# Kernel tuning notes

Hardware: AMD Instinct MI355X
Metric: run time of the kernel (lower is better)

## Reference

```python
import jax, jax.numpy as jnp
import numpy as np

RADIUS = 1
N_POINTS = 8


def lbp(x, radius=RADIUS, n_points=N_POINTS):
    """skimage-style 'default' LBP applied per pixel of an NCHW batch.

    For each of P points on a circle of radius R, bilinearly sample the
    neighbor (zero outside the image, matching skimage's constant mode),
    compare >= center, and bit-pack with weights 2**p.
    Offsets follow skimage: row = -R*sin(theta), col = R*cos(theta).
    """
    B, C, H, W = x.shape
    angles = 2.0 * np.pi * np.arange(n_points) / n_points
    drs = np.round(-radius * np.sin(angles), 8)
    dcs = np.round(radius * np.cos(angles), 8)
    pad = int(np.ceil(radius)) + 1
    xp = jnp.pad(x, ((0, 0), (0, 0), (pad, pad), (pad, pad)))  # zeros outside

    code = jnp.zeros_like(x)
    for p in range(n_points):
        dr, dc = float(drs[p]), float(dcs[p])
        r0, c0 = int(np.floor(dr)), int(np.floor(dc))
        fr, fc = dr - r0, dc - c0  # fractional parts in [0,1)

        def win(ri, ci):
            rs, cs = pad + r0 + ri, pad + c0 + ci
            return jax.lax.slice(xp, (0, 0, rs, cs), (B, C, rs + H, cs + W))

        # bilinear sample of the shifted neighborhood (constant-0 boundary)
        v = ((1 - fr) * (1 - fc) * win(0, 0)
             + (1 - fr) * fc * win(0, 1)
             + fr * (1 - fc) * win(1, 0)
             + fr * fc * win(1, 1))
        code = code + float(2 ** p) * (v >= x).astype(x.dtype)
    return code


def setup_inputs() -> dict:
    key = jax.random.key(0)
    x = jax.random.uniform(key, (16, 64, 224, 224), dtype=jnp.float32)
    return {"x": x}


def reference(x):
    return lbp(x)
```

## Files before the change

### kernel.cpp

```cpp
#include <hip/hip_runtime.h>
#include <math.h>

#define HH 224
#define WW 224
#define PLANES (16 * 64)
#define TILES_X (WW / 4)
#define TILES_PER_PLANE (TILES_X * (HH / 4))
#define TOTAL_THREADS (PLANES * TILES_PER_PLANE)

struct LbpWeights {
    float w1[4];
    float w3[4];
    float w5[4];
    float w7[4];
};

__global__ __launch_bounds__(256) void lbp_kernel(const float* __restrict__ x,
                                                  float* __restrict__ out,
                                                  LbpWeights wt) {
    int tid = blockIdx.x * 256 + threadIdx.x;

    int plane = tid / TILES_PER_PLANE;
    int t = tid - plane * TILES_PER_PLANE;
    int tr = t / TILES_X;
    int tc = t - tr * TILES_X;
    int r0 = tr * 4, c0 = tc * 4;

    const float* pb = x + (size_t)plane * (HH * WW);

    float a[6][6];
    bool cm = (c0 > 0), cp = (c0 + 4 < WW);
#pragma unroll
    for (int i = 0; i < 6; i++) {
        int rr = r0 - 1 + i;
        if (rr >= 0 && rr < HH) {
            const float* rp = pb + rr * WW + c0;
            float4 v = *(const float4*)rp;
            a[i][1] = v.x; a[i][2] = v.y; a[i][3] = v.z; a[i][4] = v.w;
            a[i][0] = cm ? rp[-1] : 0.0f;
            a[i][5] = cp ? rp[4]  : 0.0f;
        } else {
#pragma unroll
            for (int k = 0; k < 6; k++) a[i][k] = 0.0f;
        }
    }

    float* ob = out + (size_t)plane * (HH * WW) + r0 * WW + c0;

#pragma unroll
    for (int j = 0; j < 4; j++) {
        float res[4];
#pragma unroll
        for (int k = 0; k < 4; k++) {
            float ctr = a[j + 1][k + 1];
            float n00 = a[j][k],     n01 = a[j][k + 1],     n02 = a[j][k + 2];
            float n10 = a[j + 1][k],                        n12 = a[j + 1][k + 2];
            float n20 = a[j + 2][k], n21 = a[j + 2][k + 1], n22 = a[j + 2][k + 2];

            float v1, v3, v5, v7;
            {
#pragma clang fp contract(off)
                v1 = ((wt.w1[0] * n01 + wt.w1[1] * n02) + wt.w1[2] * ctr) + wt.w1[3] * n12;
                v3 = ((wt.w3[0] * n00 + wt.w3[1] * n01) + wt.w3[2] * n10) + wt.w3[3] * ctr;
                v5 = ((wt.w5[0] * n10 + wt.w5[1] * ctr) + wt.w5[2] * n20) + wt.w5[3] * n21;
                v7 = ((wt.w7[0] * ctr + wt.w7[1] * n12) + wt.w7[2] * n21) + wt.w7[3] * n22;
            }

            int m = 0;
            m |= (n12 >= ctr) ? 1   : 0;
            m |= (v1  >= ctr) ? 2   : 0;
            m |= (n01 >= ctr) ? 4   : 0;
            m |= (v3  >= ctr) ? 8   : 0;
            m |= (n10 >= ctr) ? 16  : 0;
            m |= (v5  >= ctr) ? 32  : 0;
            m |= (n21 >= ctr) ? 64  : 0;
            m |= (v7  >= ctr) ? 128 : 0;
            res[k] = (float)m;
        }
        *(float4*)(ob + j * WW) = make_float4(res[0], res[1], res[2], res[3]);
    }
}

extern "C" void kernel_launch(void* const* d_in, const int* in_sizes, int n_in,
                              void* d_out, int out_size, void* d_ws, size_t ws_size,
                              hipStream_t stream) {
    (void)in_sizes; (void)n_in; (void)d_ws; (void)ws_size; (void)out_size;
    const float* x = (const float*)d_in[0];
    float* out = (float*)d_out;

    LbpWeights wt;
    float* slots[4] = {wt.w1, wt.w3, wt.w5, wt.w7};
    const int diag_p[4] = {1, 3, 5, 7};
    for (int i = 0; i < 4; i++) {
        int p = diag_p[i];
        double ang = (2.0 * M_PI * (double)p) / 8.0;
        double dr = rint(-sin(ang) * 1e8) / 1e8;
        double dc = rint( cos(ang) * 1e8) / 1e8;
        double r0 = floor(dr), c0 = floor(dc);
        double fr = dr - r0, fc = dc - c0;
        slots[i][0] = (float)((1.0 - fr) * (1.0 - fc));
        slots[i][1] = (float)((1.0 - fr) * fc);
        slots[i][2] = (float)(fr * (1.0 - fc));
        slots[i][3] = (float)(fr * fc);
    }

    const int block = 256;
    const int grid = TOTAL_THREADS / block;
    lbp_kernel<<<grid, block, 0, stream>>>(x, out, wt);
}
```

Baseline: 371.8 us.

## Stream 28-row strips per thread with rolling row buffer and nontemporal stores

Each thread now walks a 4-wide, 28-row strip and keeps a rotating four-row register window, so every input row is loaded once per strip instead of adding halo rows to each 4x4 tile. This removes redundant halo loads, about 6/4 row reads per output row before versus roughly 30/28 now. Stores use nontemporal hints and launch bounds request higher occupancy. The cost is 7x fewer threads, so there is less parallelism for hiding latency and each thread runs a serial loop.

```diff
diff --git a/kernel.cpp b/kernel.cpp
--- a/kernel.cpp
+++ b/kernel.cpp
@@ -4,9 +4,13 @@
 #define HH 224
 #define WW 224
 #define PLANES (16 * 64)
-#define TILES_X (WW / 4)
-#define TILES_PER_PLANE (TILES_X * (HH / 4))
-#define TOTAL_THREADS (PLANES * TILES_PER_PLANE)
+#define TILES_X 56
+#define STRIPS_Y 8
+#define RSTRIP 28
+#define SPP (TILES_X * STRIPS_Y)
+#define TOTAL_THREADS (PLANES * SPP)
+
+typedef float f4v __attribute__((ext_vector_type(4)));
 
 struct LbpWeights {
     float w1[4];
@@ -15,69 +19,88 @@
     float w7[4];
 };
 
-__global__ __launch_bounds__(256) void lbp_kernel(const float* __restrict__ x,
-                                                  float* __restrict__ out,
-                                                  LbpWeights wt) {
+__device__ __forceinline__ void load_row6(const float* __restrict__ pb, int rr,
+                                          int c0, bool cm, bool cp, float w[6]) {
+    if ((unsigned)rr < (unsigned)HH) {
+        const float* rp = pb + rr * WW + c0;
+        float4 v = *(const float4*)rp;
+        w[1] = v.x; w[2] = v.y; w[3] = v.z; w[4] = v.w;
+        w[0] = cm ? rp[-1] : 0.0f;
+        w[5] = cp ? rp[4]  : 0.0f;
+    } else {
+        w[0] = w[1] = w[2] = w[3] = w[4] = w[5] = 0.0f;
+    }
+}
+
+__device__ __forceinline__ void compute_store(const float a[6], const float b[6],
+                                              const float c[6],
+                                              const LbpWeights& wt,
+                                              float* __restrict__ op) {
+    float res[4];
+#pragma unroll
+    for (int k = 0; k < 4; k++) {
+        float ctr = b[k + 1];
+        float n00 = a[k], n01 = a[k + 1], n02 = a[k + 2];
+        float n10 = b[k],                 n12 = b[k + 2];
+        float n20 = c[k], n21 = c[k + 1], n22 = c[k + 2];
+
+        float v1, v3, v5, v7;
+        {
+#pragma clang fp contract(off)
+            v1 = ((wt.w1[0] * n01 + wt.w1[1] * n02) + wt.w1[2] * ctr) + wt.w1[3] * n12;
+            v3 = ((wt.w3[0] * n00 + wt.w3[1] * n01) + wt.w3[2] * n10) + wt.w3[3] * ctr;
+            v5 = ((wt.w5[0] * n10 + wt.w5[1] * ctr) + wt.w5[2] * n20) + wt.w5[3] * n21;
+            v7 = ((wt.w7[0] * ctr + wt.w7[1] * n12) + wt.w7[2] * n21) + wt.w7[3] * n22;
+        }
+
+        int m = 0;
+        m |= (n12 >= ctr) ? 1   : 0;
+        m |= (v1  >= ctr) ? 2   : 0;
+        m |= (n01 >= ctr) ? 4   : 0;
+        m |= (v3  >= ctr) ? 8   : 0;
+        m |= (n10 >= ctr) ? 16  : 0;
+        m |= (v5  >= ctr) ? 32  : 0;
+        m |= (n21 >= ctr) ? 64  : 0;
+        m |= (v7  >= ctr) ? 128 : 0;
+        res[k] = (float)m;
+    }
+    f4v o;
+    o.x = res[0]; o.y = res[1]; o.z = res[2]; o.w = res[3];
+    __builtin_nontemporal_store(o, (f4v*)op);
+}
+
+__global__ __launch_bounds__(256, 8) void lbp_kernel(const float* __restrict__ x,
+                                                     float* __restrict__ out,
+                                                     LbpWeights wt) {
     int tid = blockIdx.x * 256 + threadIdx.x;
-
-    int plane = tid / TILES_PER_PLANE;
-    int t = tid - plane * TILES_PER_PLANE;
-    int tr = t / TILES_X;
-    int tc = t - tr * TILES_X;
-    int r0 = tr * 4, c0 = tc * 4;
+    int plane = tid / SPP;
+    int s = tid - plane * SPP;
+    int sr = s / TILES_X;
+    int tc = s - sr * TILES_X;
+    int c0 = tc * 4;
+    int r0 = sr * RSTRIP;
 
     const float* pb = x + (size_t)plane * (HH * WW);
+    float* op = out + (size_t)plane * (HH * WW) + (size_t)r0 * WW + c0;
+    bool cm = (c0 > 0), cp = (c0 + 4 < WW);
 
-    float a[6][6];
-    bool cm = (c0 > 0), cp = (c0 + 4 < WW);
-#pragma unroll
-    for (int i = 0; i < 6; i++) {
-        int rr = r0 - 1 + i;
-        if (rr >= 0 && rr < HH) {
-            const float* rp = pb + rr * WW + c0;
-            float4 v = *(const float4*)rp;
-            a[i][1] = v.x; a[i][2] = v.y; a[i][3] = v.z; a[i][4] = v.w;
-            a[i][0] = cm ? rp[-1] : 0.0f;
-            a[i][5] = cp ? rp[4]  : 0.0f;
-        } else {
-#pragma unroll
-            for (int k = 0; k < 6; k++) a[i][k] = 0.0f;
-        }
-    }
+    float w0[6], w1[6], w2[6], w3[6];
+    load_row6(pb, r0 - 1, c0, cm, cp, w0);
+    load_row6(pb, r0,     c0, cm, cp, w1);
+    load_row6(pb, r0 + 1, c0, cm, cp, w2);
 
-    float* ob = out + (size_t)plane * (HH * WW) + r0 * WW + c0;
-
-#pragma unroll
-    for (int j = 0; j < 4; j++) {
-        float res[4];
-#pragma unroll
-        for (int k = 0; k < 4; k++) {
-            float ctr = a[j + 1][k + 1];
-            float n00 = a[j][k],     n01 = a[j][k + 1],     n02 = a[j][k + 2];
-            float n10 = a[j + 1][k],                        n12 = a[j + 1][k + 2];
-            float n20 = a[j + 2][k], n21 = a[j + 2][k + 1], n22 = a[j + 2][k + 2];
-
-            float v1, v3, v5, v7;
-            {
-#pragma clang fp contract(off)
-                v1 = ((wt.w1[0] * n01 + wt.w1[1] * n02) + wt.w1[2] * ctr) + wt.w1[3] * n12;
-                v3 = ((wt.w3[0] * n00 + wt.w3[1] * n01) + wt.w3[2] * n10) + wt.w3[3] * ctr;
-                v5 = ((wt.w5[0] * n10 + wt.w5[1] * ctr) + wt.w5[2] * n20) + wt.w5[3] * n21;
-                v7 = ((wt.w7[0] * ctr + wt.w7[1] * n12) + wt.w7[2] * n21) + wt.w7[3] * n22;
-            }
-
-            int m = 0;
-            m |= (n12 >= ctr) ? 1   : 0;
-            m |= (v1  >= ctr) ? 2   : 0;
-            m |= (n01 >= ctr) ? 4   : 0;
-            m |= (v3  >= ctr) ? 8   : 0;
-            m |= (n10 >= ctr) ? 16  : 0;
-            m |= (v5  >= ctr) ? 32  : 0;
-            m |= (n21 >= ctr) ? 64  : 0;
-            m |= (v7  >= ctr) ? 128 : 0;
-            res[k] = (float)m;
-        }
-        *(float4*)(ob + j * WW) = make_float4(res[0], res[1], res[2], res[3]);
+    int r = r0;
+#pragma unroll 1
+    for (int g = 0; g < 7; ++g) {
+        load_row6(pb, r + 2, c0, cm, cp, w3);
+        compute_store(w0, w1, w2, wt, op); op += WW;
+        load_row6(pb, r + 3, c0, cm, cp, w0);
+        compute_store(w1, w2, w3, wt, op); op += WW;
+        load_row6(pb, r + 4, c0, cm, cp, w1);
+        compute_store(w2, w3, w0, wt, op); op += WW;
+        load_row6(pb, r + 5, c0, cm, cp, w2);
+        compute_store(w3, w0, w1, wt, op); op += WW;
+        r += 4;
     }
 }
 
```

Result: no change. 377.8 us (+1.6%).

## Widen LBP tiles to 4x8 and share diagonal weight products

Applied to the files above, without the earlier changes.

Each thread now computes a 4x8 output tile instead of 4x4, loading two float4 vectors per row. This cuts the halo reload ratio and the thread count. The diagonal bilinear weights are reduced to three symmetric scalars (A, B, C), so products like B*n01 and C*ctr are computed once and reused across the four diagonal samples. The change adds register pressure from the 6x10 window, and it relies on the weight symmetry reproducing the same float rounding as the original per-direction weights.

```diff
diff --git a/kernel.cpp b/kernel.cpp
--- a/kernel.cpp
+++ b/kernel.cpp
@@ -3,67 +3,75 @@
 
 #define HH 224
 #define WW 224
+#define TW 8
+#define TH 4
+#define TILES_X (WW / TW)
+#define TILES_Y (HH / TH)
+#define TPP (TILES_X * TILES_Y)
 #define PLANES (16 * 64)
-#define TILES_X (WW / 4)
-#define TILES_PER_PLANE (TILES_X * (HH / 4))
-#define TOTAL_THREADS (PLANES * TILES_PER_PLANE)
+#define TOTAL_THREADS (PLANES * TPP)
 
-struct LbpWeights {
-    float w1[4];
-    float w3[4];
-    float w5[4];
-    float w7[4];
-};
+typedef float f4v __attribute__((ext_vector_type(4)));
 
 __global__ __launch_bounds__(256) void lbp_kernel(const float* __restrict__ x,
                                                   float* __restrict__ out,
-                                                  LbpWeights wt) {
+                                                  float A, float B, float C) {
     int tid = blockIdx.x * 256 + threadIdx.x;
-
-    int plane = tid / TILES_PER_PLANE;
-    int t = tid - plane * TILES_PER_PLANE;
-    int tr = t / TILES_X;
-    int tc = t - tr * TILES_X;
-    int r0 = tr * 4, c0 = tc * 4;
+    int plane = tid / TPP;
+    int t = tid - plane * TPP;
+    int ty = t / TILES_X;
+    int tx = t - ty * TILES_X;
+    int r0 = ty * TH, c0 = tx * TW;
 
     const float* pb = x + (size_t)plane * (HH * WW);
+    bool cm = (c0 > 0), cp = (c0 + TW < WW);
+    int loff = cm ? -1 : 0;
+    int roff = cp ? TW : TW - 1;
 
-    float a[6][6];
-    bool cm = (c0 > 0), cp = (c0 + 4 < WW);
+    float w[6][10];
 #pragma unroll
     for (int i = 0; i < 6; i++) {
         int rr = r0 - 1 + i;
-        if (rr >= 0 && rr < HH) {
+        if ((unsigned)rr < (unsigned)HH) {
             const float* rp = pb + rr * WW + c0;
-            float4 v = *(const float4*)rp;
-            a[i][1] = v.x; a[i][2] = v.y; a[i][3] = v.z; a[i][4] = v.w;
-            a[i][0] = cm ? rp[-1] : 0.0f;
-            a[i][5] = cp ? rp[4]  : 0.0f;
+            f4v v0 = *(const f4v*)rp;
+            f4v v1 = *(const f4v*)(rp + 4);
+            float lv = rp[loff];
+            float rv = rp[roff];
+            w[i][0] = cm ? lv : 0.0f;
+            w[i][1] = v0.x; w[i][2] = v0.y; w[i][3] = v0.z; w[i][4] = v0.w;
+            w[i][5] = v1.x; w[i][6] = v1.y; w[i][7] = v1.z; w[i][8] = v1.w;
+            w[i][9] = cp ? rv : 0.0f;
         } else {
 #pragma unroll
-            for (int k = 0; k < 6; k++) a[i][k] = 0.0f;
+            for (int k = 0; k < 10; k++) w[i][k] = 0.0f;
         }
     }
 
-    float* ob = out + (size_t)plane * (HH * WW) + r0 * WW + c0;
+    float* ob = out + (size_t)plane * (HH * WW) + (size_t)r0 * WW + c0;
 
 #pragma unroll
-    for (int j = 0; j < 4; j++) {
-        float res[4];
+    for (int j = 0; j < TH; j++) {
+        float res[TW];
 #pragma unroll
-        for (int k = 0; k < 4; k++) {
-            float ctr = a[j + 1][k + 1];
-            float n00 = a[j][k],     n01 = a[j][k + 1],     n02 = a[j][k + 2];
-            float n10 = a[j + 1][k],                        n12 = a[j + 1][k + 2];
-            float n20 = a[j + 2][k], n21 = a[j + 2][k + 1], n22 = a[j + 2][k + 2];
+        for (int k = 0; k < TW; k++) {
+            float ctr = w[j + 1][k + 1];
+            float n00 = w[j][k],     n01 = w[j][k + 1],     n02 = w[j][k + 2];
+            float n10 = w[j + 1][k],                        n12 = w[j + 1][k + 2];
+            float n20 = w[j + 2][k], n21 = w[j + 2][k + 1], n22 = w[j + 2][k + 2];
 
             float v1, v3, v5, v7;
             {
 #pragma clang fp contract(off)
-                v1 = ((wt.w1[0] * n01 + wt.w1[1] * n02) + wt.w1[2] * ctr) + wt.w1[3] * n12;
-                v3 = ((wt.w3[0] * n00 + wt.w3[1] * n01) + wt.w3[2] * n10) + wt.w3[3] * ctr;
-                v5 = ((wt.w5[0] * n10 + wt.w5[1] * ctr) + wt.w5[2] * n20) + wt.w5[3] * n21;
-                v7 = ((wt.w7[0] * ctr + wt.w7[1] * n12) + wt.w7[2] * n21) + wt.w7[3] * n22;
+                float q   = C * ctr;
+                float b01 = B * n01;
+                float b12 = B * n12;
+                float b10 = B * n10;
+                float b21 = B * n21;
+                v1 = ((b01 + A * n02) + q) + b12;
+                v3 = ((A * n00 + b01) + b10) + q;
+                v5 = ((b10 + q) + A * n20) + b21;
+                v7 = ((q + b12) + b21) + A * n22;
             }
 
             int m = 0;
@@ -77,7 +85,11 @@
             m |= (v7  >= ctr) ? 128 : 0;
             res[k] = (float)m;
         }
-        *(float4*)(ob + j * WW) = make_float4(res[0], res[1], res[2], res[3]);
+        f4v o0, o1;
+        o0.x = res[0]; o0.y = res[1]; o0.z = res[2]; o0.w = res[3];
+        o1.x = res[4]; o1.y = res[5]; o1.z = res[6]; o1.w = res[7];
+        *(f4v*)(ob + j * WW) = o0;
+        *(f4v*)(ob + j * WW + 4) = o1;
     }
 }
 
@@ -88,23 +100,15 @@
     const float* x = (const float*)d_in[0];
     float* out = (float*)d_out;
 
-    LbpWeights wt;
-    float* slots[4] = {wt.w1, wt.w3, wt.w5, wt.w7};
-    const int diag_p[4] = {1, 3, 5, 7};
-    for (int i = 0; i < 4; i++) {
-        int p = diag_p[i];
-        double ang = (2.0 * M_PI * (double)p) / 8.0;
-        double dr = rint(-sin(ang) * 1e8) / 1e8;
-        double dc = rint( cos(ang) * 1e8) / 1e8;
-        double r0 = floor(dr), c0 = floor(dc);
-        double fr = dr - r0, fc = dc - c0;
-        slots[i][0] = (float)((1.0 - fr) * (1.0 - fc));
-        slots[i][1] = (float)((1.0 - fr) * fc);
-        slots[i][2] = (float)(fr * (1.0 - fc));
-        slots[i][3] = (float)(fr * fc);
-    }
+    double ang = 2.0 * M_PI / 8.0;
+    double dr = rint(-sin(ang) * 1e8) / 1e8;
+    double dc = rint( cos(ang) * 1e8) / 1e8;
+    double fr = dr - floor(dr), fc = dc - floor(dc);
+    float wB = (float)((1.0 - fr) * (1.0 - fc));
+    float wA = (float)((1.0 - fr) * fc);
+    float wC = (float)(fr * (1.0 - fc));
 
     const int block = 256;
     const int grid = TOTAL_THREADS / block;
-    lbp_kernel<<<grid, block, 0, stream>>>(x, out, wt);
+    lbp_kernel<<<grid, block, 0, stream>>>(x, out, wA, wB, wC);
 }
```

Measured after the change: 372.2 us. Within noise of the previous version (+0.1%).
